# Kernel tuning notes

Measured on AMD Instinct MI355X. Metric: run time of the kernel, lower is better.

## Reference

```python
import jax, jax.numpy as jnp
import numpy as np

B, T, E, H = 8, 128, 256, 256
D = E + H  # fcEnergy width = hiddenDim + embDim


def setup_inputs() -> dict:
    key = jax.random.key(0)
    ks = jax.random.split(key, 10)
    u = lambda k, shape, n: jax.random.uniform(
        k, shape, jnp.float32, -1.0 / np.sqrt(n), 1.0 / np.sqrt(n))
    lengths = jax.random.randint(ks[1], (B,), 1, T + 1)
    lengths = lengths.at[0].set(T)  # pad_sequence pads to max length == T
    return {
        "x": jax.random.normal(ks[0], (B, T, E), jnp.float32),
        "seq_lengths": lengths,
        # fcEnergy: Linear(D,D) -> Tanh -> Linear(D,1) -> Tanh
        "W1": u(ks[2], (D, D), D), "b1": u(ks[3], (D,), D),
        "W2": u(ks[4], (1, D), D), "b2": u(ks[5], (1,), D),
        # single-layer unidirectional nn.LSTM (gate order i,f,g,o)
        "Wih": u(ks[6], (4 * H, E), H), "Whh": u(ks[7], (4 * H, H), H),
        "bih": u(ks[8], (4 * H,), H), "bhh": u(ks[9], (4 * H,), H),
    }


def reference(x, seq_lengths, W1, b1, W2, b2, Wih, Whh, bih, bhh):
    Bq, Tq, _ = x.shape
    Hq = Whh.shape[1]
    jpos = jnp.arange(Tq)
    valid = jpos[None, :] < seq_lengths[:, None]  # [B,T] word validity mask
    NEG = jnp.float32(-1e30)

    def step(carry, t):
        h, c, h_last = carry  # [B,H] each
        active = t < seq_lengths  # [B] sentence still running at step t
        # attention energy over ALL words of each sentence, conditioned on h
        feat = jnp.concatenate(
            [x, jnp.broadcast_to(h[:, None, :], (Bq, Tq, Hq))], axis=-1)  # [B,T,E+H]
        hdn = jnp.tanh(jnp.einsum('btd,kd->btk', feat, W1) + b1)
        energy = jnp.tanh(jnp.einsum('btk,ok->bto', hdn, W2) + b2)[..., 0]  # [B,T]
        w = jax.nn.softmax(jnp.where(valid, energy, NEG), axis=1)
        w = jnp.where(active[:, None] & valid, w, 0.0)  # zeros for finished sentences
        context = jnp.einsum('bt,bte->be', w, x)  # [B,E] (zero when inactive)
        # one LSTM step on the context (LSTM runs for the whole batch, as in torch)
        gates = context @ Wih.T + bih + h @ Whh.T + bhh  # [B,4H]
        i, f, g, o = jnp.split(gates, 4, axis=-1)
        c_new = jax.nn.sigmoid(f) * c + jax.nn.sigmoid(i) * jnp.tanh(g)
        h_new = jax.nn.sigmoid(o) * jnp.tanh(c_new)
        # record hidden state at each sentence's last real word
        h_last = jnp.where((t == seq_lengths - 1)[:, None], h_new, h_last)
        return (h_new, c_new, h_last), (h_new, w)

    h0 = jnp.zeros((Bq, Hq), x.dtype)
    (_, _, h_last), (outs, attn) = jax.lax.scan(
        step, (h0, h0, h0), jnp.arange(Tq))
    # mask padded positions of the per-word LSTM outputs: [B,T,H]
    outputs = jnp.where(valid[..., None], outs.transpose(1, 0, 2), 0.0)
    # attention matrices A[b,i,j]: weight on word j when encoding word i
    attn = jnp.where(valid[:, :, None] & valid[:, None, :],
                     attn.transpose(1, 0, 2), 0.0)
    hidden_state = h_last[None]  # [LAYERS*DIR=1, B, H]
    return (outputs, seq_lengths, hidden_state, attn)
```

## Files before the change

kernel.cpp:

```cpp
#include <hip/hip_runtime.h>
#include <hip/hip_bf16.h>

#define B 8
#define T 128
#define E 256
#define H 256

#define LOG2E 1.4426950408889634f

#define OFF_OUT  0
#define OFF_LEN  262144
#define OFF_HID  262152
#define OFF_ATTN 264200

#define WS_XW1   0
#define WS_COMM  1048576
#define CM_PS    0
#define CM_H     1024
#define CM_CNT   1536
#define CM_GEN   1600
#define CM_STRIDE 2048

__device__ __forceinline__ float blo(unsigned int u) { return __uint_as_float(u << 16); }
__device__ __forceinline__ float bhi(unsigned int u) { return __uint_as_float(u & 0xffff0000u); }
__device__ __forceinline__ unsigned short f2bf(float f) {
    unsigned int x = __float_as_uint(f);
    return (unsigned short)((x + 0x7FFFu + ((x >> 16) & 1u)) >> 16);
}
__device__ __forceinline__ unsigned int pk(float a, float b) {
    return ((unsigned int)f2bf(b) << 16) | (unsigned int)f2bf(a);
}
__device__ __forceinline__ float fast_rcp(float x) { return __builtin_amdgcn_rcpf(x); }
__device__ __forceinline__ float fast_exp(float x) { return __builtin_amdgcn_exp2f(x * LOG2E); }
__device__ __forceinline__ float fast_tanh(float x) {
    float e = __builtin_amdgcn_exp2f(x * (2.0f * LOG2E));
    return fmaf(-2.0f, fast_rcp(1.0f + e), 1.0f);
}
__device__ __forceinline__ float fast_sigmoid(float x) {
    return fast_rcp(1.0f + __builtin_amdgcn_exp2f(-x * LOG2E));
}

__device__ __forceinline__ float ld_agent(const float* p) {
    return __hip_atomic_load(p, __ATOMIC_RELAXED, __HIP_MEMORY_SCOPE_AGENT);
}
__device__ __forceinline__ void st_agent(float* p, float v) {
    __hip_atomic_store(p, v, __ATOMIC_RELAXED, __HIP_MEMORY_SCOPE_AGENT);
}

__device__ __forceinline__ void batch_barrier(unsigned int* cnt, unsigned int* gen) {
    __syncthreads();
    if (threadIdx.x == 0) {
        asm volatile("s_waitcnt vmcnt(0) lgkmcnt(0)" ::: "memory");
        unsigned int g = __hip_atomic_load(gen, __ATOMIC_RELAXED, __HIP_MEMORY_SCOPE_AGENT);
        unsigned int old = __hip_atomic_fetch_add(cnt, 1u, __ATOMIC_RELAXED, __HIP_MEMORY_SCOPE_AGENT);
        if (old == 7u) {
            __hip_atomic_store(cnt, 0u, __ATOMIC_RELAXED, __HIP_MEMORY_SCOPE_AGENT);
            asm volatile("s_waitcnt vmcnt(0)" ::: "memory");
            __hip_atomic_fetch_add(gen, 1u, __ATOMIC_RELAXED, __HIP_MEMORY_SCOPE_AGENT);
        } else {
            while (__hip_atomic_load(gen, __ATOMIC_RELAXED, __HIP_MEMORY_SCOPE_AGENT) == g)
                __builtin_amdgcn_s_sleep(2);
        }
        asm volatile("" ::: "memory");
    }
    __syncthreads();
}

__global__ __launch_bounds__(512) void xw1_kernel(
        const float* __restrict__ x, const float* __restrict__ b1,
        const float* __restrict__ W1, unsigned short* __restrict__ Xw1bf,
        float* __restrict__ comm) {
    if (blockIdx.x == 0 && threadIdx.x < 16) {
        int bb = threadIdx.x >> 1;
        unsigned int* p = (unsigned int*)(comm + (size_t)bb * CM_STRIDE +
                                          ((threadIdx.x & 1) ? CM_GEN : CM_CNT));
        __hip_atomic_store(p, 0u, __ATOMIC_RELAXED, __HIP_MEMORY_SCOPE_AGENT);
    }
    __shared__ float xs[8 * 256];
    int b = blockIdx.x >> 4;
    int t0 = (blockIdx.x & 15) * 8;
    const float* xrow = x + (size_t)(b * T + t0) * E;
    for (int i = threadIdx.x; i < 2048; i += 512) xs[i] = xrow[i];
    __syncthreads();
    int k = threadIdx.x;
    float acc[8];
    float bk = b1[k];
#pragma unroll
    for (int r = 0; r < 8; ++r) acc[r] = bk;
    const float4* wr = (const float4*)(W1 + (size_t)k * 512);
    for (int d4 = 0; d4 < 64; ++d4) {
        float4 w = wr[d4];
        int dd = d4 * 4;
#pragma unroll
        for (int r = 0; r < 8; ++r) {
            float a = acc[r];
            a = fmaf(xs[r * 256 + dd + 0], w.x, a);
            a = fmaf(xs[r * 256 + dd + 1], w.y, a);
            a = fmaf(xs[r * 256 + dd + 2], w.z, a);
            a = fmaf(xs[r * 256 + dd + 3], w.w, a);
            acc[r] = a;
        }
    }
    unsigned short* orow = Xw1bf + (size_t)(b * T + t0) * 512 + k;
#pragma unroll
    for (int r = 0; r < 8; ++r) orow[(size_t)r * 512] = f2bf(acc[r]);
}

#define PKMAC4(wu, su) \
    a = fmaf(blo(wu.x), blo(su.x), a); a = fmaf(bhi(wu.x), bhi(su.x), a); \
    a = fmaf(blo(wu.y), blo(su.y), a); a = fmaf(bhi(wu.y), bhi(su.y), a); \
    a = fmaf(blo(wu.z), blo(su.z), a); a = fmaf(bhi(wu.z), bhi(su.z), a); \
    a = fmaf(blo(wu.w), blo(su.w), a); a = fmaf(bhi(wu.w), bhi(su.w), a);

__global__ __launch_bounds__(512) void scan_kernel(
        const int* __restrict__ seqlen, const float* __restrict__ W1,
        const float* __restrict__ W2, const float* __restrict__ b2,
        const float* __restrict__ Wih, const float* __restrict__ Whh,
        const float* __restrict__ bih, const float* __restrict__ bhh,
        const float* __restrict__ xf, const unsigned short* __restrict__ Xw1bf,
        float* __restrict__ comm, float* __restrict__ out) {
    __shared__ unsigned int lx[16384];
    __shared__ unsigned int sh_hp[128];
    __shared__ unsigned int sh_scat[272];
    __shared__ float sh_hw1l[64], sh_w2l[64];
    __shared__ float sh_en[128], sh_w[128];
    __shared__ float sh_ctxp[1024];
    __shared__ float sh_gl[128], sh_cl[32];

    const int tid = threadIdx.x;
    const int b = blockIdx.x & 7, j = blockIdx.x >> 3;
    const int lane = tid & 63, wv = tid >> 6;
    const int len = seqlen[b];
    const float b2v = b2[0];

    float* cm = comm + (size_t)b * CM_STRIDE;
    float* PSc = cm + CM_PS;
    float* Hc  = cm + CM_H;
    unsigned int* cm_cnt = (unsigned int*)(cm + CM_CNT);
    unsigned int* cm_gen = (unsigned int*)(cm + CM_GEN);

    const int kk = tid >> 3, s8 = tid & 7;
    uint4 w1q[4];
    {
        const float* w1s = W1 + (size_t)(j * 64 + kk) * 512 + 256 + s8 * 32;
#pragma unroll
        for (int c = 0; c < 4; ++c) {
            float4 f0 = *(const float4*)(w1s + c * 8);
            float4 f1 = *(const float4*)(w1s + c * 8 + 4);
            w1q[c] = make_uint4(pk(f0.x, f0.y), pk(f0.z, f0.w), pk(f1.x, f1.y), pk(f1.z, f1.w));
        }
    }
    const int tq = tid >> 2, q4 = tid & 3;
    uint4 xw0, xw1v;
    {
        const uint4* xwp = (const uint4*)(Xw1bf + ((size_t)(b * T + tq) * 512 + j * 64 + q4 * 16));
        xw0 = xwp[0]; xw1v = xwp[1];
    }
    const int rloc = tid >> 2, q3 = tid & 3;
    const int g = rloc >> 5, ii = rloc & 31;
    const int rg = g * 256 + j * 32 + ii;
    uint4 wg[16];
    {
        const float* wsrc = ((q3 < 2) ? Wih : Whh) + (size_t)rg * 256 + (q3 & 1) * 128;
#pragma unroll
        for (int c = 0; c < 16; ++c) {
            float4 f0 = *(const float4*)(wsrc + c * 8);
            float4 f1 = *(const float4*)(wsrc + c * 8 + 4);
            wg[c] = make_uint4(pk(f0.x, f0.y), pk(f0.z, f0.w), pk(f1.x, f1.y), pk(f1.z, f1.w));
        }
    }
    float bg = 0.f;
    if (q3 == 0) bg = bih[rg] + bhh[rg];

    for (int i = tid; i < 16384; i += 512) {
        int tr = i >> 7, e2 = i & 127;
        float2 v = *(const float2*)(xf + ((size_t)(b * T + tr) * 256 + e2 * 2));
        lx[tr * 128 + e2] = pk(v.x, v.y);
    }
    if (tid < 64)  sh_w2l[tid] = W2[j * 64 + tid];
    if (tid < 128) sh_hp[tid] = 0u;
    if (tid < 32)  sh_cl[tid] = 0.f;
    if (j == 0 && tid == 0) out[OFF_LEN + b] = (float)len;
    __syncthreads();

    for (int t = 0; t < len; ++t) {
        {
            const uint4* hp4 = (const uint4*)(sh_hp + s8 * 16);
            float a = 0.f;
#pragma unroll
            for (int c = 0; c < 4; ++c) {
                uint4 su = hp4[c];
                uint4 wu = w1q[c];
                PKMAC4(wu, su);
            }
            a += __shfl_xor(a, 1, 64); a += __shfl_xor(a, 2, 64); a += __shfl_xor(a, 4, 64);
            if (s8 == 0) sh_hw1l[kk] = a;
        }
        __syncthreads();
        {
            int kb = q4 * 16;
            float a;
            a  =      fast_tanh(blo(xw0.x)  + sh_hw1l[kb + 0])  * sh_w2l[kb + 0];
            a = fmaf(fast_tanh(bhi(xw0.x)  + sh_hw1l[kb + 1]),  sh_w2l[kb + 1], a);
            a = fmaf(fast_tanh(blo(xw0.y)  + sh_hw1l[kb + 2]),  sh_w2l[kb + 2], a);
            a = fmaf(fast_tanh(bhi(xw0.y)  + sh_hw1l[kb + 3]),  sh_w2l[kb + 3], a);
            a = fmaf(fast_tanh(blo(xw0.z)  + sh_hw1l[kb + 4]),  sh_w2l[kb + 4], a);
            a = fmaf(fast_tanh(bhi(xw0.z)  + sh_hw1l[kb + 5]),  sh_w2l[kb + 5], a);
            a = fmaf(fast_tanh(blo(xw0.w)  + sh_hw1l[kb + 6]),  sh_w2l[kb + 6], a);
            a = fmaf(fast_tanh(bhi(xw0.w)  + sh_hw1l[kb + 7]),  sh_w2l[kb + 7], a);
            a = fmaf(fast_tanh(blo(xw1v.x) + sh_hw1l[kb + 8]),  sh_w2l[kb + 8], a);
            a = fmaf(fast_tanh(bhi(xw1v.x) + sh_hw1l[kb + 9]),  sh_w2l[kb + 9], a);
            a = fmaf(fast_tanh(blo(xw1v.y) + sh_hw1l[kb + 10]), sh_w2l[kb + 10], a);
            a = fmaf(fast_tanh(bhi(xw1v.y) + sh_hw1l[kb + 11]), sh_w2l[kb + 11], a);
            a = fmaf(fast_tanh(blo(xw1v.z) + sh_hw1l[kb + 12]), sh_w2l[kb + 12], a);
            a = fmaf(fast_tanh(bhi(xw1v.z) + sh_hw1l[kb + 13]), sh_w2l[kb + 13], a);
            a = fmaf(fast_tanh(blo(xw1v.w) + sh_hw1l[kb + 14]), sh_w2l[kb + 14], a);
            a = fmaf(fast_tanh(bhi(xw1v.w) + sh_hw1l[kb + 15]), sh_w2l[kb + 15], a);
            a += __shfl_xor(a, 1, 64); a += __shfl_xor(a, 2, 64);
            if (q4 == 0) st_agent(&PSc[j * 128 + tq], a);
        }
        batch_barrier(cm_cnt, cm_gen);

        if (tid < 128) {
            float s = 0.f;
#pragma unroll
            for (int si = 0; si < 8; ++si) s += ld_agent(&PSc[si * 128 + tid]);
            sh_en[tid] = fast_tanh(s + b2v);
        }
        __syncthreads();
        if (wv == 0) {
            float e0 = (lane < len) ? sh_en[lane] : -1e30f;
            float e1 = (lane + 64 < len) ? sh_en[lane + 64] : -1e30f;
            float m = fmaxf(e0, e1);
#pragma unroll
            for (int off = 32; off > 0; off >>= 1) m = fmaxf(m, __shfl_xor(m, off, 64));
            float p0 = (lane < len) ? fast_exp(e0 - m) : 0.f;
            float p1 = (lane + 64 < len) ? fast_exp(e1 - m) : 0.f;
            float s = p0 + p1;
#pragma unroll
            for (int off = 32; off > 0; off >>= 1) s += __shfl_xor(s, off, 64);
            float rs = fast_rcp(s);
            float w0 = p0 * rs, w1 = p1 * rs;
            sh_w[lane] = w0; sh_w[lane + 64] = w1;
            if (j == 0) {
                float* arow = out + OFF_ATTN + ((size_t)b * T + t) * T;
                arow[lane] = w0; arow[lane + 64] = w1;
            }
        }
        __syncthreads();
        {
            int q = tid >> 7, e2 = tid & 127;
            float a0 = 0.f, a1 = 0.f;
#pragma unroll 8
            for (int i5 = 0; i5 < 32; ++i5) {
                int tp = q * 32 + i5;
                unsigned int u = lx[tp * 128 + e2];
                float wv2 = sh_w[tp];
                a0 = fmaf(blo(u), wv2, a0);
                a1 = fmaf(bhi(u), wv2, a1);
            }
            sh_ctxp[q * 256 + e2] = a0;
            sh_ctxp[q * 256 + 128 + e2] = a1;
        }
        __syncthreads();
        if (tid < 128) {
            float ev = sh_ctxp[tid] + sh_ctxp[256 + tid] + sh_ctxp[512 + tid] + sh_ctxp[768 + tid];
            float ov = sh_ctxp[128 + tid] + sh_ctxp[384 + tid] + sh_ctxp[640 + tid] + sh_ctxp[896 + tid];
            sh_scat[(tid >> 6) * 68 + (tid & 63)] = pk(ev, ov);
        } else if (tid < 256) {
            sh_scat[(tid >> 6) * 68 + (tid & 63)] = sh_hp[tid - 128];
        }
        __syncthreads();
        {
            const uint4* sp = (const uint4*)(sh_scat + q3 * 68);
            float a = 0.f;
#pragma unroll
            for (int c = 0; c < 16; ++c) {
                uint4 su = sp[c];
                uint4 wu = wg[c];
                PKMAC4(wu, su);
            }
            a += __shfl_xor(a, 1, 64); a += __shfl_xor(a, 2, 64);
            if (q3 == 0) sh_gl[rloc] = a + bg;
        }
        __syncthreads();
        if (tid < 32) {
            float gi = sh_gl[tid], gf = sh_gl[32 + tid];
            float gg = sh_gl[64 + tid], go = sh_gl[96 + tid];
            float cn = fast_sigmoid(gf) * sh_cl[tid] + fast_sigmoid(gi) * fast_tanh(gg);
            float hn = fast_sigmoid(go) * fast_tanh(cn);
            sh_cl[tid] = cn;
            int hidx = j * 32 + tid;
            out[OFF_OUT + ((size_t)b * T + t) * H + hidx] = hn;
            if (t == len - 1) out[OFF_HID + b * H + hidx] = hn;
            st_agent(&Hc[hidx], hn);
        }
        batch_barrier(cm_cnt, cm_gen);
        if (tid < 128) {
            float lo = ld_agent(&Hc[2 * tid]);
            float hi = ld_agent(&Hc[2 * tid + 1]);
            sh_hp[tid] = pk(lo, hi);
        }
        __syncthreads();
    }

    for (int tt = len + j; tt < T; tt += 8) {
        for (int i = tid; i < H; i += 512) out[OFF_OUT + ((size_t)b * T + tt) * H + i] = 0.f;
        for (int i = tid; i < T; i += 512) out[OFF_ATTN + ((size_t)b * T + tt) * T + i] = 0.f;
    }
}

extern "C" void kernel_launch(void* const* d_in, const int* in_sizes, int n_in,
                              void* d_out, int out_size, void* d_ws, size_t ws_size,
                              hipStream_t stream) {
    const float* x   = (const float*)d_in[0];
    const int*   sl  = (const int*)  d_in[1];
    const float* W1  = (const float*)d_in[2];
    const float* b1  = (const float*)d_in[3];
    const float* W2  = (const float*)d_in[4];
    const float* b2  = (const float*)d_in[5];
    const float* Wih = (const float*)d_in[6];
    const float* Whh = (const float*)d_in[7];
    const float* bih = (const float*)d_in[8];
    const float* bhh = (const float*)d_in[9];

    char* ws = (char*)d_ws;
    unsigned short* Xw1  = (unsigned short*)(ws + WS_XW1);
    float*          comm = (float*)(ws + WS_COMM);
    float* out = (float*)d_out;

    hipLaunchKernelGGL(xw1_kernel, dim3(128), dim3(512), 0, stream, x, b1, W1, Xw1, comm);

    void* args[] = {(void*)&sl, (void*)&W1, (void*)&W2, (void*)&b2, (void*)&Wih,
                    (void*)&Whh, (void*)&bih, (void*)&bhh, (void*)&x, (void*)&Xw1,
                    (void*)&comm, (void*)&out};
    hipLaunchCooperativeKernel((const void*)scan_kernel, dim3(64), dim3(512), args, 0, stream);
}
```

Before: 944.1 us.

## Replace counter barriers with epoch-tagged 64-bit flag-data exchange between blocks

Removes the two per-step atomic counter/generation barriers across the 8 blocks of each batch. Each block now writes its partial energies and packed hidden state as 64-bit words holding the step epoch in the high half and the payload in the low half. Readers spin until every word they need carries the current epoch, so no separate barrier round-trip is required. The workspace zeroing is widened to clear the whole comm region. In exchange, 128 threads poll global memory, and correctness relies on 64-bit atomic stores being single-copy atomic and on the epoch never repeating within a launch.

```diff
diff --git a/kernel.cpp b/kernel.cpp
--- a/kernel.cpp
+++ b/kernel.cpp
@@ -15,11 +15,9 @@
 
 #define WS_XW1   0
 #define WS_COMM  1048576
-#define CM_PS    0
-#define CM_H     1024
-#define CM_CNT   1536
-#define CM_GEN   1600
-#define CM_STRIDE 2048
+#define CM_U64_STRIDE 2048
+
+typedef unsigned long long u64t;
 
 __device__ __forceinline__ float blo(unsigned int u) { return __uint_as_float(u << 16); }
 __device__ __forceinline__ float bhi(unsigned int u) { return __uint_as_float(u & 0xffff0000u); }
@@ -40,42 +38,19 @@
     return fast_rcp(1.0f + __builtin_amdgcn_exp2f(-x * LOG2E));
 }
 
-__device__ __forceinline__ float ld_agent(const float* p) {
+__device__ __forceinline__ u64t ld64(const u64t* p) {
     return __hip_atomic_load(p, __ATOMIC_RELAXED, __HIP_MEMORY_SCOPE_AGENT);
 }
-__device__ __forceinline__ void st_agent(float* p, float v) {
+__device__ __forceinline__ void st64(u64t* p, u64t v) {
     __hip_atomic_store(p, v, __ATOMIC_RELAXED, __HIP_MEMORY_SCOPE_AGENT);
-}
-
-__device__ __forceinline__ void batch_barrier(unsigned int* cnt, unsigned int* gen) {
-    __syncthreads();
-    if (threadIdx.x == 0) {
-        asm volatile("s_waitcnt vmcnt(0) lgkmcnt(0)" ::: "memory");
-        unsigned int g = __hip_atomic_load(gen, __ATOMIC_RELAXED, __HIP_MEMORY_SCOPE_AGENT);
-        unsigned int old = __hip_atomic_fetch_add(cnt, 1u, __ATOMIC_RELAXED, __HIP_MEMORY_SCOPE_AGENT);
-        if (old == 7u) {
-            __hip_atomic_store(cnt, 0u, __ATOMIC_RELAXED, __HIP_MEMORY_SCOPE_AGENT);
-            asm volatile("s_waitcnt vmcnt(0)" ::: "memory");
-            __hip_atomic_fetch_add(gen, 1u, __ATOMIC_RELAXED, __HIP_MEMORY_SCOPE_AGENT);
-        } else {
-            while (__hip_atomic_load(gen, __ATOMIC_RELAXED, __HIP_MEMORY_SCOPE_AGENT) == g)
-                __builtin_amdgcn_s_sleep(2);
-        }
-        asm volatile("" ::: "memory");
-    }
-    __syncthreads();
 }
 
 __global__ __launch_bounds__(512) void xw1_kernel(
         const float* __restrict__ x, const float* __restrict__ b1,
         const float* __restrict__ W1, unsigned short* __restrict__ Xw1bf,
-        float* __restrict__ comm) {
-    if (blockIdx.x == 0 && threadIdx.x < 16) {
-        int bb = threadIdx.x >> 1;
-        unsigned int* p = (unsigned int*)(comm + (size_t)bb * CM_STRIDE +
-                                          ((threadIdx.x & 1) ? CM_GEN : CM_CNT));
-        __hip_atomic_store(p, 0u, __ATOMIC_RELAXED, __HIP_MEMORY_SCOPE_AGENT);
-    }
+        u64t* __restrict__ commz) {
+    int gid = blockIdx.x * 512 + threadIdx.x;
+    if (gid < 8 * CM_U64_STRIDE) commz[gid] = 0ull;
     __shared__ float xs[8 * 256];
     int b = blockIdx.x >> 4;
     int t0 = (blockIdx.x & 15) * 8;
@@ -118,7 +93,7 @@
         const float* __restrict__ Wih, const float* __restrict__ Whh,
         const float* __restrict__ bih, const float* __restrict__ bhh,
         const float* __restrict__ xf, const unsigned short* __restrict__ Xw1bf,
-        float* __restrict__ comm, float* __restrict__ out) {
+        u64t* __restrict__ comm, float* __restrict__ out) {
     __shared__ unsigned int lx[16384];
     __shared__ unsigned int sh_hp[128];
     __shared__ unsigned int sh_scat[272];
@@ -133,11 +108,9 @@
     const int len = seqlen[b];
     const float b2v = b2[0];
 
-    float* cm = comm + (size_t)b * CM_STRIDE;
-    float* PSc = cm + CM_PS;
-    float* Hc  = cm + CM_H;
-    unsigned int* cm_cnt = (unsigned int*)(cm + CM_CNT);
-    unsigned int* cm_gen = (unsigned int*)(cm + CM_GEN);
+    u64t* cmb = comm + (size_t)b * CM_U64_STRIDE;
+    u64t* PSp = cmb;
+    u64t* Hp  = cmb + 1024;
 
     const int kk = tid >> 3, s8 = tid & 7;
     uint4 w1q[4];
@@ -184,6 +157,7 @@
     __syncthreads();
 
     for (int t = 0; t < len; ++t) {
+        const unsigned int ep = (unsigned int)(t + 1);
         {
             const uint4* hp4 = (const uint4*)(sh_hp + s8 * 16);
             float a = 0.f;
@@ -217,15 +191,24 @@
             a = fmaf(fast_tanh(blo(xw1v.w) + sh_hw1l[kb + 14]), sh_w2l[kb + 14], a);
             a = fmaf(fast_tanh(bhi(xw1v.w) + sh_hw1l[kb + 15]), sh_w2l[kb + 15], a);
             a += __shfl_xor(a, 1, 64); a += __shfl_xor(a, 2, 64);
-            if (q4 == 0) st_agent(&PSc[j * 128 + tq], a);
-        }
-        batch_barrier(cm_cnt, cm_gen);
-
+            if (q4 == 0)
+                st64(&PSp[j * 128 + tq], ((u64t)ep << 32) | (u64t)__float_as_uint(a));
+        }
         if (tid < 128) {
-            float s = 0.f;
-#pragma unroll
-            for (int si = 0; si < 8; ++si) s += ld_agent(&PSc[si * 128 + tid]);
-            sh_en[tid] = fast_tanh(s + b2v);
+            u64t v[8];
+            bool ok;
+            do {
+#pragma unroll
+                for (int s = 0; s < 8; ++s) v[s] = ld64(&PSp[s * 128 + tid]);
+                ok = true;
+#pragma unroll
+                for (int s = 0; s < 8; ++s) ok = ok && ((unsigned int)(v[s] >> 32) == ep);
+            } while (!ok);
+            asm volatile("" ::: "memory");
+            float s2 = 0.f;
+#pragma unroll
+            for (int s = 0; s < 8; ++s) s2 += __uint_as_float((unsigned int)v[s]);
+            sh_en[tid] = fast_tanh(s2 + b2v);
         }
         __syncthreads();
         if (wv == 0) {
@@ -284,22 +267,28 @@
             if (q3 == 0) sh_gl[rloc] = a + bg;
         }
         __syncthreads();
-        if (tid < 32) {
-            float gi = sh_gl[tid], gf = sh_gl[32 + tid];
-            float gg = sh_gl[64 + tid], go = sh_gl[96 + tid];
-            float cn = fast_sigmoid(gf) * sh_cl[tid] + fast_sigmoid(gi) * fast_tanh(gg);
-            float hn = fast_sigmoid(go) * fast_tanh(cn);
-            sh_cl[tid] = cn;
-            int hidx = j * 32 + tid;
-            out[OFF_OUT + ((size_t)b * T + t) * H + hidx] = hn;
-            if (t == len - 1) out[OFF_HID + b * H + hidx] = hn;
-            st_agent(&Hc[hidx], hn);
-        }
-        batch_barrier(cm_cnt, cm_gen);
+        if (wv == 0) {
+            float hn = 0.f;
+            if (lane < 32) {
+                float gi = sh_gl[lane], gf = sh_gl[32 + lane];
+                float gg = sh_gl[64 + lane], go = sh_gl[96 + lane];
+                float cn = fast_sigmoid(gf) * sh_cl[lane] + fast_sigmoid(gi) * fast_tanh(gg);
+                hn = fast_sigmoid(go) * fast_tanh(cn);
+                sh_cl[lane] = cn;
+                int hidx = j * 32 + lane;
+                out[OFF_OUT + ((size_t)b * T + t) * H + hidx] = hn;
+                if (t == len - 1) out[OFF_HID + b * H + hidx] = hn;
+            }
+            float h0 = __shfl(hn, (lane & 15) * 2, 64);
+            float h1 = __shfl(hn, (lane & 15) * 2 + 1, 64);
+            if (lane < 16)
+                st64(&Hp[j * 16 + lane], ((u64t)ep << 32) | (u64t)pk(h0, h1));
+        }
         if (tid < 128) {
-            float lo = ld_agent(&Hc[2 * tid]);
-            float hi = ld_agent(&Hc[2 * tid + 1]);
-            sh_hp[tid] = pk(lo, hi);
+            u64t hv;
+            do { hv = ld64(&Hp[tid]); } while ((unsigned int)(hv >> 32) != ep);
+            asm volatile("" ::: "memory");
+            sh_hp[tid] = (unsigned int)hv;
         }
         __syncthreads();
     }
@@ -326,7 +315,7 @@
 
     char* ws = (char*)d_ws;
     unsigned short* Xw1  = (unsigned short*)(ws + WS_XW1);
-    float*          comm = (float*)(ws + WS_COMM);
+    u64t*           comm = (u64t*)(ws + WS_COMM);
     float* out = (float*)d_out;
 
     hipLaunchKernelGGL(xw1_kernel, dim3(128), dim3(512), 0, stream, x, b1, W1, Xw1, comm);
```

Result: faster. 764.2 us (-19.1%).
